# Performance work log

Measured on AMD Instinct MI355X. Metric: run time of the kernel, lower is better.

The kernel has to match this reference:

```python
import jax, jax.numpy as jnp
import numpy as np

H, D = 4, 32
EMB = H * D  # 128
COUNTS = [30000, 20000, 25000, 50000]  # pesticide, disease, plant, event
EDGE_TYPES = [(0, 1), (1, 0), (2, 1), (1, 2), (3, 0), (0, 3), (3, 2), (2, 3)]
E = 200000
INV_SQRT_D = 1.0 / float(np.sqrt(D))


def layer_norm(x, g, b, eps=1e-5):
    m = x.mean(-1, keepdims=True)
    v = ((x - m) ** 2).mean(-1, keepdims=True)
    return (x - m) * jax.lax.rsqrt(v + eps) * g + b


def hgt_block(xs, edges, kqvW, kqvb, outW, outb, skip, a_rel, m_rel, p_rel, ln_g, ln_b):
    # type-specific K/Q/V projections -> [N, H, D]
    K, Q, V = [], [], []
    for t in range(4):
        kqv = jnp.einsum('nc,kdc->knd', xs[t], kqvW[t]) + kqvb[t][:, None, :]
        K.append(kqv[0].reshape(-1, H, D))
        Q.append(kqv[1].reshape(-1, H, D))
        V.append(kqv[2].reshape(-1, H, D))
    per_dst = {t: [] for t in range(4)}
    for r, (s, t) in enumerate(EDGE_TYPES):
        src, dst = edges[r, 0], edges[r, 1]
        k_rel = jnp.einsum('ehd,hdf->ehf', K[s][src], a_rel[r])  # relation-specific key transform
        v_rel = jnp.einsum('ehd,hdf->ehf', V[s][src], m_rel[r])  # relation-specific message transform
        logit = (k_rel * Q[t][dst]).sum(-1) * p_rel[r] * INV_SQRT_D  # [E, H]
        per_dst[t].append((logit, v_rel, dst))
    outs = []
    for t in range(4):
        N = xs[t].shape[0]
        logits = jnp.concatenate([p[0] for p in per_dst[t]], axis=0)
        vals = jnp.concatenate([p[1] for p in per_dst[t]], axis=0)
        idx = jnp.concatenate([p[2] for p in per_dst[t]], axis=0)
        # single segment softmax per destination node across ALL incoming edge types (PyG HGTConv)
        mx = jax.ops.segment_max(logits, idx, num_segments=N)
        ex = jnp.exp(logits - mx[idx])
        den = jax.ops.segment_sum(ex, idx, num_segments=N)
        alpha = ex / jnp.maximum(den[idx], 1e-16)
        agg = jax.ops.segment_sum(vals * alpha[..., None], idx, num_segments=N).reshape(N, EMB)
        o = jax.nn.gelu(agg, approximate=False) @ outW[t].T + outb[t]
        sg = jax.nn.sigmoid(skip[t])
        o = sg * o + (1.0 - sg) * xs[t]  # HGTConv learnable skip
        # HGTBlock: residual add, LayerNorm, ReLU (dropout = identity in eval)
        outs.append(jax.nn.relu(layer_norm(o + xs[t], ln_g, ln_b)))
    return outs


def fusion(seq, inW, inb, outW, outb, g, b):
    # seq: [N, 3, EMB]; torch MultiheadAttention self-attention, then mean + LN
    qkv = seq @ inW.T + inb  # [N, 3, 3*EMB]
    q, k, v = jnp.split(qkv, 3, axis=-1)
    heads = lambda x: x.reshape(x.shape[0], 3, H, D).transpose(0, 2, 1, 3)  # [N,H,3,D]
    q, k, v = heads(q), heads(k), heads(v)
    att = jax.nn.softmax(jnp.einsum('nhqd,nhkd->nhqk', q, k) * INV_SQRT_D, axis=-1)
    o = jnp.einsum('nhqk,nhkd->nhqd', att, v).transpose(0, 2, 1, 3).reshape(-1, 3, EMB)
    o = o @ outW.T + outb
    return layer_norm(o.mean(axis=1), g, b)


def _forward(x_pest, x_dis, x_plant, edges, proj_W, proj_b, event_emb, kqv_W, kqv_b,
             out_W, out_b, skip, a_rel, m_rel, p_rel, blk_ln_g, blk_ln_b,
             fin_W, fin_b, fout_W, fout_b, f_ln_g, f_ln_b):
    xs = [jax.nn.relu(x_pest @ proj_W[0].T + proj_b[0]),
          jax.nn.relu(x_dis @ proj_W[1].T + proj_b[1]),
          jax.nn.relu(x_plant @ proj_W[2].T + proj_b[2]),
          event_emb]  # event_emb(arange(N)) == the full table
    layers = []
    cur = xs
    for l in range(3):
        cur = hgt_block(cur, edges, kqv_W[l], kqv_b[l], out_W[l], out_b[l], skip[l],
                        a_rel[l], m_rel[l], p_rel[l], blk_ln_g[l], blk_ln_b[l])
        layers.append(cur)
    outs = []
    for j, t in enumerate([0, 1, 2]):  # pesticide, disease, plant
        seq = jnp.stack([layers[0][t], layers[1][t], layers[2][t]], axis=1)
        outs.append(fusion(seq, fin_W[j], fin_b[j], fout_W[j], fout_b[j], f_ln_g[j], f_ln_b[j]))
    return jnp.concatenate(outs, axis=0)  # [30000+20000+25000, 128]


def setup_inputs() -> dict:
    key = jax.random.key(0)
    ks = iter(jax.random.split(key, 64))
    nrm = lambda shape, s=0.05: jax.random.normal(next(ks), shape, dtype=jnp.float32) * s
    rows = []
    for s, t in EDGE_TYPES:
        rows.append(jnp.stack([jax.random.randint(next(ks), (E,), 0, COUNTS[s]),
                               jax.random.randint(next(ks), (E,), 0, COUNTS[t])]))
    return {
        'x_pest': nrm((COUNTS[0], 64), 1.0),
        'x_dis': nrm((COUNTS[1], 64), 1.0),
        'x_plant': nrm((COUNTS[2], 64), 1.0),
        'edges': jnp.stack(rows).astype(jnp.int32),  # [8, 2, E]
        'proj_W': nrm((3, EMB, 64)), 'proj_b': nrm((3, EMB)),
        'event_emb': nrm((COUNTS[3], EMB), 1.0),
        'kqv_W': nrm((3, 4, 3, EMB, EMB)), 'kqv_b': nrm((3, 4, 3, EMB)),
        'out_W': nrm((3, 4, EMB, EMB)), 'out_b': nrm((3, 4, EMB)),
        'skip': nrm((3, 4), 1.0),
        'a_rel': nrm((3, 8, H, D, D), 0.1), 'm_rel': nrm((3, 8, H, D, D), 0.1),
        'p_rel': jnp.ones((3, 8, H), jnp.float32),
        'blk_ln_g': jnp.ones((3, EMB), jnp.float32), 'blk_ln_b': jnp.zeros((3, EMB), jnp.float32),
        'fin_W': nrm((3, 3 * EMB, EMB)), 'fin_b': nrm((3, 3 * EMB)),
        'fout_W': nrm((3, EMB, EMB)), 'fout_b': nrm((3, EMB)),
        'f_ln_g': jnp.ones((3, EMB), jnp.float32), 'f_ln_b': jnp.zeros((3, EMB), jnp.float32),
    }


def reference(x_pest, x_dis, x_plant, edges, proj_W, proj_b, event_emb, kqv_W, kqv_b,
              out_W, out_b, skip, a_rel, m_rel, p_rel, blk_ln_g, blk_ln_b,
              fin_W, fin_b, fout_W, fout_b, f_ln_g, f_ln_b):
    return _forward(x_pest, x_dis, x_plant, edges, proj_W, proj_b, event_emb, kqv_W, kqv_b,
                    out_W, out_b, skip, a_rel, m_rel, p_rel, blk_ln_g, blk_ln_b,
                    fin_W, fin_b, fout_W, fout_b, f_ln_g, f_ln_b)
```

## Files before the change

### kernel.cpp

```cpp
#include <hip/hip_runtime.h>
#include <math.h>

#define E_CNT 200000
typedef unsigned short bfu;
typedef unsigned short u16;
typedef __attribute__((ext_vector_type(8))) short bh8;
typedef __attribute__((ext_vector_type(4))) float f4;

__device__ __forceinline__ float gelu_f(float x) {
    return 0.5f * x * (1.0f + erff(x * 0.70710678118654752f));
}
__device__ __forceinline__ float bf2f(bfu u) { return __uint_as_float(((unsigned)u) << 16); }
__device__ __forceinline__ bfu f2bf(float f) {
    unsigned u = __float_as_uint(f);
    unsigned r = u + 0x7FFFu + ((u >> 16) & 1u);
    return (bfu)(r >> 16);
}
__device__ __forceinline__ int rsrc_of(int r) {
    const int a[8] = {0, 1, 2, 1, 3, 0, 3, 2}; return a[r];
}
__device__ __forceinline__ int rdst_of(int r) {
    const int a[8] = {1, 0, 1, 2, 0, 3, 2, 3}; return a[r];
}
__device__ __forceinline__ int rpoff_of(int r) {
    const int a[9] = {0, 20001, 50002, 70003, 95004, 125005, 175006, 200007, 250008};
    return a[r];
}

__global__ __launch_bounds__(256) void fill_val(float* p, int n, float v) {
    int i = blockIdx.x * 256 + threadIdx.x;
    if (i < n) p[i] = v;
}

__global__ __launch_bounds__(256) void cvt_pack(
    const float* __restrict__ out_W, const float* __restrict__ kqv_W,
    const float* __restrict__ fin_W, const float* __restrict__ fout_W,
    const float* __restrict__ event_emb,
    bfu* __restrict__ OWB, bfu* __restrict__ KWB, bfu* __restrict__ FINWB,
    bfu* __restrict__ FOUTWB, bfu* __restrict__ EVB)
{
    int i = blockIdx.x * 256 + threadIdx.x;
    const float* src; bfu* dst; size_t so, dox;
    if (i < 49152) { src = out_W; dst = OWB; so = (size_t)i * 4; dox = so; }
    else if (i < 98304) {
        int j = i - 49152; int m = j >> 12; int o = (j & 4095) * 4;
        src = kqv_W; dst = KWB;
        so = (size_t)m * 3 * 16384 + o; dox = (size_t)m * 16384 + o;
    }
    else if (i < 135168) { int j = i - 98304; src = fin_W; dst = FINWB; so = (size_t)j * 4; dox = so; }
    else if (i < 147456) { int j = i - 135168; src = fout_W; dst = FOUTWB; so = (size_t)j * 4; dox = so; }
    else if (i < 1747456) { int j = i - 147456; src = event_emb; dst = EVB; so = (size_t)j * 4; dox = so; }
    else return;
    float4 v = *(const float4*)(src + so);
    uint2 u;
    u.x = ((unsigned)f2bf(v.x)) | (((unsigned)f2bf(v.y)) << 16);
    u.y = ((unsigned)f2bf(v.z)) | (((unsigned)f2bf(v.w)) << 16);
    *(uint2*)(dst + dox) = u;
}

__global__ __launch_bounds__(256) void hist_all(const int* __restrict__ edges, int* __restrict__ rp) {
    int i = blockIdx.x * 256 + threadIdx.x;
    if (i >= 8 * E_CNT) return;
    int r = i / E_CNT, e = i - r * E_CNT;
    int d = edges[(size_t)(2 * r + 1) * E_CNT + e];
    atomicAdd(&rp[rpoff_of(r) + d + 1], 1);
}
__global__ __launch_bounds__(1024) void scan_part(int* __restrict__ a, int* __restrict__ part, int n) {
    __shared__ int lds[1024];
    int t = threadIdx.x, i = blockIdx.x * 1024 + t;
    int v = (i < n) ? a[i] : 0;
    lds[t] = v;
    __syncthreads();
    for (int off = 1; off < 1024; off <<= 1) {
        int u = (t >= off) ? lds[t - off] : 0;
        __syncthreads();
        lds[t] += u;
        __syncthreads();
    }
    if (i < n) a[i] = lds[t];
    if (t == 1023) part[blockIdx.x] = lds[1023];
}
__global__ __launch_bounds__(256) void scan_tot(int* __restrict__ part, int nb) {
    __shared__ int lds[256];
    int t = threadIdx.x;
    int v = (t < nb) ? part[t] : 0;
    lds[t] = v;
    __syncthreads();
    for (int off = 1; off < 256; off <<= 1) {
        int u = (t >= off) ? lds[t - off] : 0;
        __syncthreads();
        lds[t] += u;
        __syncthreads();
    }
    if (t < nb) part[t] = lds[t];
}
__global__ __launch_bounds__(1024) void scan_add(int* __restrict__ a, const int* __restrict__ part, int n) {
    int b = blockIdx.x + 1;
    int i = b * 1024 + threadIdx.x;
    if (i < n) a[i] += part[b - 1];
}
__global__ __launch_bounds__(256) void scatter_all(
    const int* __restrict__ edges, const int* __restrict__ RP,
    int* __restrict__ cur, u16* __restrict__ SIDX) {
    int i = blockIdx.x * 256 + threadIdx.x;
    if (i >= 8 * E_CNT) return;
    int r = i / E_CNT, e = i - r * E_CNT;
    int d = edges[(size_t)(2 * r + 1) * E_CNT + e];
    int pos = RP[rpoff_of(r) + d] + atomicAdd(&cur[r * 50000 + d], 1);
    SIDX[pos] = (u16)edges[(size_t)(2 * r) * E_CNT + e];
}

__global__ __launch_bounds__(256) void proj_gemm(
    const float* __restrict__ X, const float* __restrict__ W,
    const float* __restrict__ bias, bfu* __restrict__ Y, int N)
{
    __shared__ __align__(16) float Wt[32][132];
    __shared__ __align__(16) float Xt[32][36];
    const int tid = threadIdx.x;
    const int r0 = blockIdx.x * 32;
    const int rg = tid >> 5, cg = tid & 31;
    float acc[4][4];
    #pragma unroll
    for (int i = 0; i < 4; ++i)
        #pragma unroll
        for (int j = 0; j < 4; ++j) acc[i][j] = 0.f;
    for (int c0 = 0; c0 < 64; c0 += 32) {
        __syncthreads();
        #pragma unroll
        for (int k = 0; k < 4; ++k) {
            int v = tid + k * 256;
            int j = v >> 3, c4 = (v & 7) * 4;
            float4 w = *(const float4*)(W + (size_t)j * 64 + c0 + c4);
            Wt[c4 + 0][j] = w.x; Wt[c4 + 1][j] = w.y;
            Wt[c4 + 2][j] = w.z; Wt[c4 + 3][j] = w.w;
        }
        {
            int rr = tid >> 3, c4 = (tid & 7) * 4;
            int row = r0 + rr;
            float4 x = make_float4(0.f, 0.f, 0.f, 0.f);
            if (row < N) x = *(const float4*)(X + (size_t)row * 64 + c0 + c4);
            Xt[c4 + 0][rr] = x.x; Xt[c4 + 1][rr] = x.y;
            Xt[c4 + 2][rr] = x.z; Xt[c4 + 3][rr] = x.w;
        }
        __syncthreads();
        #pragma unroll
        for (int cc = 0; cc < 32; ++cc) {
            float4 xv = *(const float4*)(&Xt[cc][rg * 4]);
            float4 wv = *(const float4*)(&Wt[cc][cg * 4]);
            #pragma unroll
            for (int i = 0; i < 4; ++i) {
                float xs = (i == 0) ? xv.x : (i == 1) ? xv.y : (i == 2) ? xv.z : xv.w;
                acc[i][0] = fmaf(xs, wv.x, acc[i][0]);
                acc[i][1] = fmaf(xs, wv.y, acc[i][1]);
                acc[i][2] = fmaf(xs, wv.z, acc[i][2]);
                acc[i][3] = fmaf(xs, wv.w, acc[i][3]);
            }
        }
    }
    float4 bv = *(const float4*)(bias + cg * 4);
    #pragma unroll
    for (int ri = 0; ri < 4; ++ri) {
        int row = r0 + rg * 4 + ri;
        if (row >= N) continue;
        float y0 = fmaxf(acc[ri][0] + bv.x, 0.f);
        float y1 = fmaxf(acc[ri][1] + bv.y, 0.f);
        float y2 = fmaxf(acc[ri][2] + bv.z, 0.f);
        float y3 = fmaxf(acc[ri][3] + bv.w, 0.f);
        uint2 u;
        u.x = ((unsigned)f2bf(y0)) | (((unsigned)f2bf(y1)) << 16);
        u.y = ((unsigned)f2bf(y2)) | (((unsigned)f2bf(y3)) << 16);
        *(uint2*)(Y + (size_t)row * 128 + cg * 4) = u;
    }
}

__global__ __launch_bounds__(256) void build_rel(
    const float* __restrict__ kqvW_l, const float* __restrict__ kqvb_l,
    const float* __restrict__ a_l, const float* __restrict__ m_l,
    bfu* __restrict__ WQAB, float* __restrict__ BQA,
    bfu* __restrict__ WVMB, float* __restrict__ BVM)
{
    __shared__ float As[32][33];
    __shared__ float Ws[32][129];
    int tid = threadIdx.x;
    int b = blockIdx.x;
    if (b < 32) {
        int r = b >> 2, h = b & 3;
        int dt = rdst_of(r);
        const float* Wq = kqvW_l + ((size_t)dt * 3 + 1) * 16384;
        const float* bq = kqvb_l + ((size_t)dt * 3 + 1) * 128;
        const float* A = a_l + (size_t)r * 4096 + h * 1024;
        for (int v = tid; v < 1024; v += 256) As[v >> 5][v & 31] = A[v];
        for (int v = tid; v < 4096; v += 256)
            Ws[v >> 7][v & 127] = Wq[(size_t)(h * 32 + (v >> 7)) * 128 + (v & 127)];
        __syncthreads();
        int c = tid & 127, half = tid >> 7;
        for (int d = half; d < 32; d += 2) {
            float acc = 0.f;
            #pragma unroll
            for (int f = 0; f < 32; ++f) acc = fmaf(As[d][f], Ws[f][c], acc);
            WQAB[((size_t)r * 128 + h * 32 + d) * 128 + c] = f2bf(acc);
        }
        if (tid < 32) {
            int d = tid;
            float acc = 0.f;
            #pragma unroll
            for (int f = 0; f < 32; ++f) acc = fmaf(As[d][f], bq[h * 32 + f], acc);
            BQA[(size_t)r * 128 + h * 32 + d] = acc;
        }
    } else {
        int bb2 = b - 32;
        int r = bb2 >> 2, h = bb2 & 3;
        int st = rsrc_of(r);
        const float* Wv = kqvW_l + ((size_t)st * 3 + 2) * 16384;
        const float* bv = kqvb_l + ((size_t)st * 3 + 2) * 128;
        const float* M = m_l + (size_t)r * 4096 + h * 1024;
        for (int v = tid; v < 1024; v += 256) As[v >> 5][v & 31] = M[v];
        for (int v = tid; v < 4096; v += 256)
            Ws[v >> 7][v & 127] = Wv[(size_t)(h * 32 + (v >> 7)) * 128 + (v & 127)];
        __syncthreads();
        int c = tid & 127, half = tid >> 7;
        for (int f = half; f < 32; f += 2) {
            float acc = 0.f;
            #pragma unroll
            for (int d = 0; d < 32; ++d) acc = fmaf(As[d][f], Ws[d][c], acc);
            WVMB[((size_t)r * 128 + h * 32 + f) * 128 + c] = f2bf(acc);
        }
        if (tid < 32) {
            int f = tid;
            float acc = 0.f;
            #pragma unroll
            for (int d = 0; d < 32; ++d) acc = fmaf(As[d][f], bv[h * 32 + d], acc);
            BVM[(size_t)r * 128 + h * 32 + f] = acc;
        }
    }
}

struct GDesc { const bfu* X; const bfu* W; const float* bias; bfu* Y; int N; int ldy; int bend; };
struct GBatch { GDesc d[9]; };

__global__ __launch_bounds__(256) void mgemm_batch(GBatch gb) {
    int b = blockIdx.x;
    int gi = 0;
    #pragma unroll
    for (int k = 0; k < 8; ++k) gi += (b >= gb.d[k].bend) ? 1 : 0;
    const bfu* X = gb.d[0].X; const bfu* W = gb.d[0].W;
    const float* bi = gb.d[0].bias; bfu* Y = gb.d[0].Y;
    int N = gb.d[0].N, ldy = gb.d[0].ldy, bstart = 0;
    #pragma unroll
    for (int k = 1; k < 9; ++k) {
        if (gi == k) {
            X = gb.d[k].X; W = gb.d[k].W; bi = gb.d[k].bias; Y = gb.d[k].Y;
            N = gb.d[k].N; ldy = gb.d[k].ldy; bstart = gb.d[k - 1].bend;
        }
    }
    int bloc = b - bstart;
    const int tid = threadIdx.x;
    const int wave = tid >> 6, lane = tid & 63;
    const int row16 = lane & 15, kgrp = lane >> 4;
    const int r_base = bloc * 128 + wave * 32;
    f4 acc[2][8];
    #pragma unroll
    for (int t = 0; t < 2; ++t)
        #pragma unroll
        for (int n = 0; n < 8; ++n) acc[t][n] = (f4){0.f, 0.f, 0.f, 0.f};
    bh8 az = {0, 0, 0, 0, 0, 0, 0, 0};
    #pragma unroll
    for (int kb = 0; kb < 4; ++kb) {
        int ar0 = r_base + row16, ar1 = r_base + 16 + row16;
        bh8 a0 = az, a1 = az;
        if (ar0 < N) a0 = *(const bh8*)(X + (size_t)ar0 * 128 + kb * 32 + kgrp * 8);
        if (ar1 < N) a1 = *(const bh8*)(X + (size_t)ar1 * 128 + kb * 32 + kgrp * 8);
        #pragma unroll
        for (int n = 0; n < 8; ++n) {
            bh8 bv = *(const bh8*)(W + (size_t)(n * 16 + row16) * 128 + kb * 32 + kgrp * 8);
            acc[0][n] = __builtin_amdgcn_mfma_f32_16x16x32_bf16(a0, bv, acc[0][n], 0, 0, 0);
            acc[1][n] = __builtin_amdgcn_mfma_f32_16x16x32_bf16(a1, bv, acc[1][n], 0, 0, 0);
        }
    }
    #pragma unroll
    for (int t = 0; t < 2; ++t) {
        const int crow0 = r_base + t * 16 + kgrp * 4;
        #pragma unroll
        for (int n = 0; n < 8; ++n) {
            int col = n * 16 + row16;
            float bn = bi[col];
            #pragma unroll
            for (int j = 0; j < 4; ++j) {
                int row = crow0 + j;
                if (row < N) Y[(size_t)row * ldy + col] = f2bf(acc[t][n][j] + bn);
            }
        }
    }
}

__global__ __launch_bounds__(256) void agg_dual(
    const bfu* QAA, const bfu* __restrict__ QAB,
    const bfu* __restrict__ KA, const bfu* __restrict__ VMA,
    const bfu* __restrict__ KB, const bfu* __restrict__ VMB,
    const int* __restrict__ rpA, const int* __restrict__ rpB,
    const u16* __restrict__ sidx,
    const float* __restrict__ prlA, const float* __restrict__ prlB,
    bfu* ACC, int Nn)
{
    int n = blockIdx.x * 4 + (threadIdx.x >> 6);
    if (n >= Nn) return;
    int l = threadIdx.x & 63;
    int h = l >> 4;
    const float scl = 0.17677669529663687f;

    float m = -3.0e38f, d = 0.f, a0 = 0.f, a1 = 0.f;

    auto upd = [&](float s, unsigned vu) {
        float nm = fmaxf(m, s);
        float sc = __expf(m - nm), w = __expf(s - nm);
        d = d * sc + w;
        a0 = fmaf(w, bf2f((bfu)vu), a0 * sc);
        a1 = fmaf(w, bf2f((bfu)(vu >> 16)), a1 * sc);
        m = nm;
    };

    {
        unsigned qu = *(const unsigned*)(QAA + (size_t)n * 128 + 2 * l);
        float q0 = bf2f((bfu)qu), q1 = bf2f((bfu)(qu >> 16));
        float ph = prlA[h] * scl;
        int i = rpA[n], e1 = rpA[n + 1];
        for (; i + 1 < e1; i += 2) {
            int sa = sidx[i], sb = sidx[i + 1];
            unsigned ka = *(const unsigned*)(KA + (size_t)sa * 128 + 2 * l);
            unsigned kb = *(const unsigned*)(KA + (size_t)sb * 128 + 2 * l);
            unsigned va = *(const unsigned*)(VMA + (size_t)sa * 128 + 2 * l);
            unsigned vb = *(const unsigned*)(VMA + (size_t)sb * 128 + 2 * l);
            float s0 = fmaf(bf2f((bfu)ka), q0, bf2f((bfu)(ka >> 16)) * q1);
            float s1 = fmaf(bf2f((bfu)kb), q0, bf2f((bfu)(kb >> 16)) * q1);
            #pragma unroll
            for (int off = 1; off <= 8; off <<= 1) {
                s0 += __shfl_xor(s0, off);
                s1 += __shfl_xor(s1, off);
            }
            upd(s0 * ph, va);
            upd(s1 * ph, vb);
        }
        if (i < e1) {
            int sa = sidx[i];
            unsigned ka = *(const unsigned*)(KA + (size_t)sa * 128 + 2 * l);
            unsigned va = *(const unsigned*)(VMA + (size_t)sa * 128 + 2 * l);
            float s0 = fmaf(bf2f((bfu)ka), q0, bf2f((bfu)(ka >> 16)) * q1);
            #pragma unroll
            for (int off = 1; off <= 8; off <<= 1) s0 += __shfl_xor(s0, off);
            upd(s0 * ph, va);
        }
    }
    {
        unsigned qu = *(const unsigned*)(QAB + (size_t)n * 128 + 2 * l);
        float q0 = bf2f((bfu)qu), q1 = bf2f((bfu)(qu >> 16));
        float ph = prlB[h] * scl;
        int i = rpB[n], e1 = rpB[n + 1];
        for (; i + 1 < e1; i += 2) {
            int sa = sidx[i], sb = sidx[i + 1];
            unsigned ka = *(const unsigned*)(KB + (size_t)sa * 128 + 2 * l);
            unsigned kb = *(const unsigned*)(KB + (size_t)sb * 128 + 2 * l);
            unsigned va = *(const unsigned*)(VMB + (size_t)sa * 128 + 2 * l);
            unsigned vb = *(const unsigned*)(VMB + (size_t)sb * 128 + 2 * l);
            float s0 = fmaf(bf2f((bfu)ka), q0, bf2f((bfu)(ka >> 16)) * q1);
            float s1 = fmaf(bf2f((bfu)kb), q0, bf2f((bfu)(kb >> 16)) * q1);
            #pragma unroll
            for (int off = 1; off <= 8; off <<= 1) {
                s0 += __shfl_xor(s0, off);
                s1 += __shfl_xor(s1, off);
            }
            upd(s0 * ph, va);
            upd(s1 * ph, vb);
        }
        if (i < e1) {
            int sa = sidx[i];
            unsigned ka = *(const unsigned*)(KB + (size_t)sa * 128 + 2 * l);
            unsigned va = *(const unsigned*)(VMB + (size_t)sa * 128 + 2 * l);
            float s0 = fmaf(bf2f((bfu)ka), q0, bf2f((bfu)(ka >> 16)) * q1);
            #pragma unroll
            for (int off = 1; off <= 8; off <<= 1) s0 += __shfl_xor(s0, off);
            upd(s0 * ph, va);
        }
    }
    float rd = 1.f / fmaxf(d, 1e-16f);
    float y0 = gelu_f(a0 * rd);
    float y1 = gelu_f(a1 * rd);
    unsigned ou = ((unsigned)f2bf(y0)) | (((unsigned)f2bf(y1)) << 16);
    *(unsigned*)(ACC + (size_t)n * 128 + 2 * l) = ou;
}

__global__ __launch_bounds__(256) void mgemm_epi_layer(
    const bfu* __restrict__ A, const bfu* __restrict__ W, const float* __restrict__ bias,
    const bfu* __restrict__ Xr, const float* __restrict__ skp,
    const float* __restrict__ g, const float* __restrict__ bb,
    bfu* __restrict__ Y, int N)
{
    const int tid = threadIdx.x;
    const int wave = tid >> 6, lane = tid & 63;
    const int row16 = lane & 15, kgrp = lane >> 4;
    const int r_base = blockIdx.x * 64 + wave * 16;
    const int arow = r_base + row16;
    f4 acc[8];
    #pragma unroll
    for (int n = 0; n < 8; ++n) acc[n] = (f4){0.f, 0.f, 0.f, 0.f};
    bh8 az = {0, 0, 0, 0, 0, 0, 0, 0};
    #pragma unroll
    for (int kb = 0; kb < 4; ++kb) {
        bh8 a = az;
        if (arow < N) a = *(const bh8*)(A + (size_t)arow * 128 + kb * 32 + kgrp * 8);
        #pragma unroll
        for (int n = 0; n < 8; ++n) {
            bh8 bv = *(const bh8*)(W + (size_t)(n * 16 + row16) * 128 + kb * 32 + kgrp * 8);
            acc[n] = __builtin_amdgcn_mfma_f32_16x16x32_bf16(a, bv, acc[n], 0, 0, 0);
        }
    }
    const int crow0 = r_base + kgrp * 4;
    float sg = 1.f / (1.f + expf(-skp[0]));
    float z[8][4];
    #pragma unroll
    for (int n = 0; n < 8; ++n) {
        float bn = bias[n * 16 + row16];
        #pragma unroll
        for (int j = 0; j < 4; ++j) z[n][j] = acc[n][j] + bn;
    }
    #pragma unroll
    for (int j = 0; j < 4; ++j) {
        int row = crow0 + j;
        if (row >= N) continue;
        #pragma unroll
        for (int n = 0; n < 8; ++n) {
            float xr = bf2f(Xr[(size_t)row * 128 + n * 16 + row16]);
            z[n][j] = sg * z[n][j] + (1.f - sg) * xr + xr;
        }
    }
    float s[4], q[4];
    #pragma unroll
    for (int j = 0; j < 4; ++j) {
        s[j] = 0.f; q[j] = 0.f;
        #pragma unroll
        for (int n = 0; n < 8; ++n) { s[j] += z[n][j]; q[j] += z[n][j] * z[n][j]; }
    }
    #pragma unroll
    for (int off = 1; off <= 8; off <<= 1) {
        #pragma unroll
        for (int j = 0; j < 4; ++j) {
            s[j] += __shfl_xor(s[j], off);
            q[j] += __shfl_xor(q[j], off);
        }
    }
    #pragma unroll
    for (int j = 0; j < 4; ++j) {
        int row = crow0 + j;
        if (row >= N) continue;
        float mean = s[j] * (1.f / 128.f);
        float var = q[j] * (1.f / 128.f) - mean * mean;
        float inv = rsqrtf(var + 1e-5f);
        #pragma unroll
        for (int n = 0; n < 8; ++n) {
            int col = n * 16 + row16;
            float y = (z[n][j] - mean) * inv * g[col] + bb[col];
            Y[(size_t)row * 128 + col] = f2bf(fmaxf(y, 0.f));
        }
    }
}

__global__ __launch_bounds__(256) void mgemm_epi_ln(
    const bfu* __restrict__ X, const bfu* __restrict__ W, const float* __restrict__ bias,
    const float* __restrict__ g, const float* __restrict__ bb,
    float* __restrict__ Y, int N)
{
    const int tid = threadIdx.x;
    const int wave = tid >> 6, lane = tid & 63;
    const int row16 = lane & 15, kgrp = lane >> 4;
    const int r_base = blockIdx.x * 64 + wave * 16;
    const int arow = r_base + row16;
    f4 acc[8];
    #pragma unroll
    for (int n = 0; n < 8; ++n) acc[n] = (f4){0.f, 0.f, 0.f, 0.f};
    bh8 az = {0, 0, 0, 0, 0, 0, 0, 0};
    #pragma unroll
    for (int kb = 0; kb < 4; ++kb) {
        bh8 a = az;
        if (arow < N) a = *(const bh8*)(X + (size_t)arow * 128 + kb * 32 + kgrp * 8);
        #pragma unroll
        for (int n = 0; n < 8; ++n) {
            bh8 bv = *(const bh8*)(W + (size_t)(n * 16 + row16) * 128 + kb * 32 + kgrp * 8);
            acc[n] = __builtin_amdgcn_mfma_f32_16x16x32_bf16(a, bv, acc[n], 0, 0, 0);
        }
    }
    const int crow0 = r_base + kgrp * 4;
    float z[8][4];
    #pragma unroll
    for (int n = 0; n < 8; ++n) {
        float bn = bias[n * 16 + row16];
        #pragma unroll
        for (int j = 0; j < 4; ++j) z[n][j] = acc[n][j] + bn;
    }
    float s[4], q[4];
    #pragma unroll
    for (int j = 0; j < 4; ++j) {
        s[j] = 0.f; q[j] = 0.f;
        #pragma unroll
        for (int n = 0; n < 8; ++n) { s[j] += z[n][j]; q[j] += z[n][j] * z[n][j]; }
    }
    #pragma unroll
    for (int off = 1; off <= 8; off <<= 1) {
        #pragma unroll
        for (int j = 0; j < 4; ++j) {
            s[j] += __shfl_xor(s[j], off);
            q[j] += __shfl_xor(q[j], off);
        }
    }
    #pragma unroll
    for (int j = 0; j < 4; ++j) {
        int row = crow0 + j;
        if (row >= N) continue;
        float mean = s[j] * (1.f / 128.f);
        float var = q[j] * (1.f / 128.f) - mean * mean;
        float inv = rsqrtf(var + 1e-5f);
        #pragma unroll
        for (int n = 0; n < 8; ++n) {
            int col = n * 16 + row16;
            Y[(size_t)row * 128 + col] = (z[n][j] - mean) * inv * g[col] + bb[col];
        }
    }
}

__global__ __launch_bounds__(256) void attn_fuse(
    const bfu* __restrict__ QKV, bfu* __restrict__ OM, int M)
{
    int n = blockIdx.x * 4 + (threadIdx.x >> 6);
    int l = threadIdx.x & 63;
    if (n >= M) return;
    const bfu* base = QKV + (size_t)n * 1152;
    float q[3][2], k[3][2], v[3][2];
    #pragma unroll
    for (int p = 0; p < 3; ++p) {
        q[p][0] = bf2f(base[(0 * 3 + p) * 128 + l]);
        q[p][1] = bf2f(base[(0 * 3 + p) * 128 + l + 64]);
        k[p][0] = bf2f(base[(1 * 3 + p) * 128 + l]);
        k[p][1] = bf2f(base[(1 * 3 + p) * 128 + l + 64]);
        v[p][0] = bf2f(base[(2 * 3 + p) * 128 + l]);
        v[p][1] = bf2f(base[(2 * 3 + p) * 128 + l + 64]);
    }
    float lgA[3][3], lgB[3][3];
    #pragma unroll
    for (int qi = 0; qi < 3; ++qi)
        #pragma unroll
        for (int ki = 0; ki < 3; ++ki) {
            float s0 = q[qi][0] * k[ki][0];
            float s1 = q[qi][1] * k[ki][1];
            #pragma unroll
            for (int off = 1; off <= 16; off <<= 1) {
                s0 += __shfl_xor(s0, off);
                s1 += __shfl_xor(s1, off);
            }
            lgA[qi][ki] = s0 * 0.17677669529663687f;
            lgB[qi][ki] = s1 * 0.17677669529663687f;
        }
    float oA = 0.f, oB = 0.f;
    #pragma unroll
    for (int qi = 0; qi < 3; ++qi) {
        float mA = fmaxf(lgA[qi][0], fmaxf(lgA[qi][1], lgA[qi][2]));
        float e0 = __expf(lgA[qi][0] - mA), e1 = __expf(lgA[qi][1] - mA), e2 = __expf(lgA[qi][2] - mA);
        float rd = 1.f / (e0 + e1 + e2);
        oA += (e0 * v[0][0] + e1 * v[1][0] + e2 * v[2][0]) * rd;
        float mB = fmaxf(lgB[qi][0], fmaxf(lgB[qi][1], lgB[qi][2]));
        float f0 = __expf(lgB[qi][0] - mB), f1 = __expf(lgB[qi][1] - mB), f2 = __expf(lgB[qi][2] - mB);
        float rdB = 1.f / (f0 + f1 + f2);
        oB += (f0 * v[0][1] + f1 * v[1][1] + f2 * v[2][1]) * rdB;
    }
    OM[(size_t)n * 128 + l] = f2bf(oA * (1.f / 3.f));
    OM[(size_t)n * 128 + l + 64] = f2bf(oB * (1.f / 3.f));
}

extern "C" void kernel_launch(void* const* d_in, const int* in_sizes, int n_in,
                              void* d_out, int out_size, void* d_ws, size_t ws_size,
                              hipStream_t stream)
{
    const float* x_pest   = (const float*)d_in[0];
    const float* x_dis    = (const float*)d_in[1];
    const float* x_plant  = (const float*)d_in[2];
    const int*   edges    = (const int*)d_in[3];
    const float* proj_W   = (const float*)d_in[4];
    const float* proj_b   = (const float*)d_in[5];
    const float* event_emb= (const float*)d_in[6];
    const float* kqv_W    = (const float*)d_in[7];
    const float* kqv_b    = (const float*)d_in[8];
    const float* out_W    = (const float*)d_in[9];
    const float* out_b    = (const float*)d_in[10];
    const float* skip     = (const float*)d_in[11];
    const float* a_rel    = (const float*)d_in[12];
    const float* m_rel    = (const float*)d_in[13];
    const float* p_rel    = (const float*)d_in[14];
    const float* blk_ln_g = (const float*)d_in[15];
    const float* blk_ln_b = (const float*)d_in[16];
    const float* fin_W    = (const float*)d_in[17];
    const float* fin_b    = (const float*)d_in[18];
    const float* fout_W   = (const float*)d_in[19];
    const float* fout_b   = (const float*)d_in[20];
    const float* f_ln_g   = (const float*)d_in[21];
    const float* f_ln_b   = (const float*)d_in[22];
    float* out = (float*)d_out;

    static const int NT[4]  = {30000, 20000, 25000, 50000};
    static const int OFF[4] = {0, 30000, 50000, 75000};
    static const int RPOFF[9] = {0, 20001, 50002, 70003, 95004, 125005, 175006, 200007, 250008};
    static const int DG[4][2][2] = { {{1,1},{4,3}}, {{0,0},{2,2}}, {{3,1},{6,3}}, {{5,0},{7,2}} };

    char* wsb = (char*)d_ws;
    size_t ob = 0;
    auto alc = [&](size_t bytes) -> void* {
        void* p = wsb + ob; ob += (bytes + 255) & ~(size_t)255; return p;
    };
    bfu* LK0  = (bfu*)alc((size_t)75000 * 128 * 2);
    bfu* LK1  = (bfu*)alc((size_t)75000 * 128 * 2);
    bfu* POOL = (bfu*)alc((size_t)210000 * 128 * 2);
    bfu* WQAB = (bfu*)alc((size_t)8 * 16384 * 2);
    float* BQA = (float*)alc((size_t)8 * 128 * 4);
    bfu* WVMB = (bfu*)alc((size_t)8 * 16384 * 2);
    float* BVM = (float*)alc((size_t)8 * 128 * 4);
    bfu* KWB  = (bfu*)alc((size_t)12 * 16384 * 2);
    bfu* OWB  = (bfu*)alc((size_t)12 * 16384 * 2);
    bfu* FINWB = (bfu*)alc((size_t)3 * 49152 * 2);
    bfu* FOUTWB = (bfu*)alc((size_t)3 * 16384 * 2);
    int* RP   = (int*)alc((size_t)250008 * 4);
    int* PART = (int*)alc(1024);
    u16* SIDX = (u16*)alc((size_t)8 * E_CNT * 2);
    if (ws_size < ob) {
        fill_val<<<(out_size + 255) / 256, 256, 0, stream>>>(out, out_size, 1e30f);
        return;
    }
    int* CUR = (int*)POOL;
    bfu* QKVf = POOL;
    bfu* OMB  = POOL + (size_t)20000 * 1152;

    bfu* EVB = (bfu*)out;
    bfu* XB  = (bfu*)((char*)out + 12800000);
    bfu* L2F = (bfu*)((char*)out + 19200000);

    cvt_pack<<<(1747456 + 255) / 256, 256, 0, stream>>>(
        out_W, kqv_W, fin_W, fout_W, event_emb, OWB, KWB, FINWB, FOUTWB, EVB);

    hipMemsetAsync(RP, 0, (size_t)250008 * 4, stream);
    const int eg8 = (8 * E_CNT + 255) / 256;
    hist_all<<<eg8, 256, 0, stream>>>(edges, RP);
    scan_part<<<245, 1024, 0, stream>>>(RP, PART, 250008);
    scan_tot<<<1, 256, 0, stream>>>(PART, 245);
    scan_add<<<244, 1024, 0, stream>>>(RP, PART, 250008);
    hipMemsetAsync(CUR, 0, (size_t)8 * 50000 * 4, stream);
    scatter_all<<<eg8, 256, 0, stream>>>(edges, RP, CUR, SIDX);

    const float* xin0[3] = {x_pest, x_dis, x_plant};
    for (int t = 0; t < 3; ++t) {
        proj_gemm<<<(NT[t] + 31) / 32, 256, 0, stream>>>(
            xin0[t], proj_W + (size_t)t * 8192, proj_b + (size_t)t * 128,
            XB + (size_t)OFF[t] * 128, NT[t]);
    }

    auto launch_batch = [&](GDesc* ds, int cnt) {
        GBatch gb;
        int acc = 0;
        for (int i = 0; i < cnt; ++i) {
            gb.d[i] = ds[i];
            acc += (ds[i].N + 127) / 128;
            gb.d[i].bend = acc;
        }
        for (int i = cnt; i < 9; ++i) { gb.d[i] = gb.d[cnt - 1]; gb.d[i].bend = acc; }
        mgemm_batch<<<acc, 256, 0, stream>>>(gb);
    };

    for (int l = 0; l < 3; ++l) {
        const float* kqvW_l = kqv_W + (size_t)l * 12 * 16384;
        const float* kqvb_l = kqv_b + (size_t)l * 12 * 128;
        build_rel<<<64, 256, 0, stream>>>(kqvW_l, kqvb_l,
            a_rel + (size_t)l * 8 * 4096, m_rel + (size_t)l * 8 * 4096,
            WQAB, BQA, WVMB, BVM);

        auto feat_ptr = [&](int tt) -> const bfu* {
            if (tt == 3) return EVB;
            if (l == 0) return XB + (size_t)OFF[tt] * 128;
            return (l == 1 ? LK0 : LK1) + (size_t)OFF[tt] * 128;
        };

        int nord = (l == 2) ? 3 : 4;
        for (int dt = 0; dt < nord; ++dt) {
            int Ndt = NT[dt];
            int rA = DG[dt][0][0], sA = DG[dt][0][1];
            int rB = DG[dt][1][0], sB = DG[dt][1][1];
            int NsA = NT[sA], NsB = NT[sB];
            bfu* QA_A = POOL;
            bfu* QA_B = QA_A + (size_t)Ndt * 128;
            bfu* K_A  = QA_B + (size_t)Ndt * 128;
            bfu* VM_A = K_A + (size_t)NsA * 128;
            bfu* K_B  = VM_A + (size_t)NsA * 128;
            bfu* VM_B = K_B + (size_t)NsB * 128;

            GDesc ds[6];
            ds[0] = { feat_ptr(dt), WQAB + (size_t)rA * 16384, BQA + (size_t)rA * 128, QA_A, Ndt, 128, 0 };
            ds[1] = { feat_ptr(dt), WQAB + (size_t)rB * 16384, BQA + (size_t)rB * 128, QA_B, Ndt, 128, 0 };
            ds[2] = { feat_ptr(sA), KWB + (size_t)(l * 4 + sA) * 16384,
                      kqvb_l + ((size_t)sA * 3 + 0) * 128, K_A, NsA, 128, 0 };
            ds[3] = { feat_ptr(sA), WVMB + (size_t)rA * 16384, BVM + (size_t)rA * 128, VM_A, NsA, 128, 0 };
            ds[4] = { feat_ptr(sB), KWB + (size_t)(l * 4 + sB) * 16384,
                      kqvb_l + ((size_t)sB * 3 + 0) * 128, K_B, NsB, 128, 0 };
            ds[5] = { feat_ptr(sB), WVMB + (size_t)rB * 16384, BVM + (size_t)rB * 128, VM_B, NsB, 128, 0 };
            launch_batch(ds, 6);

            agg_dual<<<(Ndt + 3) / 4, 256, 0, stream>>>(
                QA_A, QA_B, K_A, VM_A, K_B, VM_B,
                RP + RPOFF[rA], RP + RPOFF[rB], SIDX,
                p_rel + (size_t)(l * 8 + rA) * 4, p_rel + (size_t)(l * 8 + rB) * 4,
                QA_A , Ndt);

            size_t wi = (size_t)l * 4 + dt;
            const bfu* xr = feat_ptr(dt);
            bfu* ydst = (dt == 3) ? EVB :
                        (l == 0 ? LK0 : (l == 1 ? LK1 : L2F)) + (size_t)OFF[dt] * 128;
            mgemm_epi_layer<<<(Ndt + 63) / 64, 256, 0, stream>>>(
                QA_A, OWB + wi * 16384, out_b + wi * 128, xr, skip + wi,
                blk_ln_g + (size_t)l * 128, blk_ln_b + (size_t)l * 128, ydst, Ndt);
        }
    }

    const int CH = 20000;
    for (int j = 0; j < 3; ++j) {
        int Nj = NT[j];
        for (int b0 = 0; b0 < Nj; b0 += CH) {
            int M = min(CH, Nj - b0);
            const bfu* srcs[3] = {
                LK0 + (size_t)(OFF[j] + b0) * 128,
                LK1 + (size_t)(OFF[j] + b0) * 128,
                L2F + (size_t)(OFF[j] + b0) * 128 };
            GDesc ds[9];
            int di = 0;
            for (int kk = 0; kk < 3; ++kk)
                for (int p = 0; p < 3; ++p) {
                    ds[di++] = { srcs[p], FINWB + (size_t)j * 49152 + (size_t)kk * 16384,
                                 fin_b + (size_t)j * 384 + kk * 128,
                                 QKVf + (size_t)(kk * 3 + p) * 128, M, 1152, 0 };
                }
            launch_batch(ds, 9);
            attn_fuse<<<(M + 3) / 4, 256, 0, stream>>>(QKVf, OMB, M);
            mgemm_epi_ln<<<(M + 63) / 64, 256, 0, stream>>>(
                OMB, FOUTWB + (size_t)j * 16384, fout_b + (size_t)j * 128,
                f_ln_g + (size_t)j * 128, f_ln_b + (size_t)j * 128,
                out + (size_t)(OFF[j] + b0) * 128, M);
        }
    }
}
```

Before: 1.802 ms.

## Batch input projections into one bf16 MFMA kernel and unroll edge loop by four

The three per-type fp32 LDS-tiled projection GEMMs become a single batched launch that uses bf16 MFMA 16x16x32, with proj_W converted to bf16 inside cvt_pack. The edge-attention kernel's two duplicated per-relation loops are folded into one lambda, and its gather loop is unrolled from two to four edges to raise memory-level parallelism. In exchange, X is rounded to bf16 before the projection, which adds precision loss, and the wider unroll raises register pressure.

After: 1.702 ms. 5.6% less time.

```diff
diff --git a/kernel.cpp b/kernel.cpp
--- a/kernel.cpp
+++ b/kernel.cpp
@@ -35,9 +35,9 @@
 __global__ __launch_bounds__(256) void cvt_pack(
     const float* __restrict__ out_W, const float* __restrict__ kqv_W,
     const float* __restrict__ fin_W, const float* __restrict__ fout_W,
-    const float* __restrict__ event_emb,
+    const float* __restrict__ event_emb, const float* __restrict__ proj_W,
     bfu* __restrict__ OWB, bfu* __restrict__ KWB, bfu* __restrict__ FINWB,
-    bfu* __restrict__ FOUTWB, bfu* __restrict__ EVB)
+    bfu* __restrict__ FOUTWB, bfu* __restrict__ EVB, bfu* __restrict__ PJWB)
 {
     int i = blockIdx.x * 256 + threadIdx.x;
     const float* src; bfu* dst; size_t so, dox;
@@ -50,6 +50,7 @@
     else if (i < 135168) { int j = i - 98304; src = fin_W; dst = FINWB; so = (size_t)j * 4; dox = so; }
     else if (i < 147456) { int j = i - 135168; src = fout_W; dst = FOUTWB; so = (size_t)j * 4; dox = so; }
     else if (i < 1747456) { int j = i - 147456; src = event_emb; dst = EVB; so = (size_t)j * 4; dox = so; }
+    else if (i < 1753600) { int j = i - 1747456; src = proj_W; dst = PJWB; so = (size_t)j * 4; dox = so; }
     else return;
     float4 v = *(const float4*)(src + so);
     uint2 u;
@@ -110,66 +111,71 @@
     SIDX[pos] = (u16)edges[(size_t)(2 * r) * E_CNT + e];
 }
 
-__global__ __launch_bounds__(256) void proj_gemm(
-    const float* __restrict__ X, const float* __restrict__ W,
-    const float* __restrict__ bias, bfu* __restrict__ Y, int N)
-{
-    __shared__ __align__(16) float Wt[32][132];
-    __shared__ __align__(16) float Xt[32][36];
+struct PDesc { const float* X; const bfu* W; const float* bias; bfu* Y; int N; int bend; };
+struct PBatch { PDesc d[3]; };
+
+__global__ __launch_bounds__(256) void mgemm_proj(PBatch pb) {
+    int b = blockIdx.x;
+    int gi = 0;
+    #pragma unroll
+    for (int k = 0; k < 2; ++k) gi += (b >= pb.d[k].bend) ? 1 : 0;
+    const float* X = pb.d[0].X; const bfu* W = pb.d[0].W;
+    const float* bi = pb.d[0].bias; bfu* Y = pb.d[0].Y;
+    int N = pb.d[0].N, bstart = 0;
+    #pragma unroll
+    for (int k = 1; k < 3; ++k) {
+        if (gi == k) {
+            X = pb.d[k].X; W = pb.d[k].W; bi = pb.d[k].bias; Y = pb.d[k].Y;
+            N = pb.d[k].N; bstart = pb.d[k - 1].bend;
+        }
+    }
+    int bloc = b - bstart;
     const int tid = threadIdx.x;
-    const int r0 = blockIdx.x * 32;
-    const int rg = tid >> 5, cg = tid & 31;
-    float acc[4][4];
-    #pragma unroll
-    for (int i = 0; i < 4; ++i)
-        #pragma unroll
-        for (int j = 0; j < 4; ++j) acc[i][j] = 0.f;
-    for (int c0 = 0; c0 < 64; c0 += 32) {
-        __syncthreads();
-        #pragma unroll
-        for (int k = 0; k < 4; ++k) {
-            int v = tid + k * 256;
-            int j = v >> 3, c4 = (v & 7) * 4;
-            float4 w = *(const float4*)(W + (size_t)j * 64 + c0 + c4);
-            Wt[c4 + 0][j] = w.x; Wt[c4 + 1][j] = w.y;
-            Wt[c4 + 2][j] = w.z; Wt[c4 + 3][j] = w.w;
-        }
-        {
-            int rr = tid >> 3, c4 = (tid & 7) * 4;
-            int row = r0 + rr;
-            float4 x = make_float4(0.f, 0.f, 0.f, 0.f);
-            if (row < N) x = *(const float4*)(X + (size_t)row * 64 + c0 + c4);
-            Xt[c4 + 0][rr] = x.x; Xt[c4 + 1][rr] = x.y;
-            Xt[c4 + 2][rr] = x.z; Xt[c4 + 3][rr] = x.w;
-        }
-        __syncthreads();
-        #pragma unroll
-        for (int cc = 0; cc < 32; ++cc) {
-            float4 xv = *(const float4*)(&Xt[cc][rg * 4]);
-            float4 wv = *(const float4*)(&Wt[cc][cg * 4]);
-            #pragma unroll
-            for (int i = 0; i < 4; ++i) {
-                float xs = (i == 0) ? xv.x : (i == 1) ? xv.y : (i == 2) ? xv.z : xv.w;
-                acc[i][0] = fmaf(xs, wv.x, acc[i][0]);
-                acc[i][1] = fmaf(xs, wv.y, acc[i][1]);
-                acc[i][2] = fmaf(xs, wv.z, acc[i][2]);
-                acc[i][3] = fmaf(xs, wv.w, acc[i][3]);
+    const int wave = tid >> 6, lane = tid & 63;
+    const int row16 = lane & 15, kgrp = lane >> 4;
+    const int r_base = bloc * 128 + wave * 32;
+    f4 acc[2][8];
+    #pragma unroll
+    for (int t = 0; t < 2; ++t)
+        #pragma unroll
+        for (int n = 0; n < 8; ++n) acc[t][n] = (f4){0.f, 0.f, 0.f, 0.f};
+    bh8 az = {0, 0, 0, 0, 0, 0, 0, 0};
+    #pragma unroll
+    for (int kb = 0; kb < 2; ++kb) {
+        bh8 a[2] = {az, az};
+        #pragma unroll
+        for (int t = 0; t < 2; ++t) {
+            int ar = r_base + t * 16 + row16;
+            if (ar < N) {
+                const float* xp = X + (size_t)ar * 64 + kb * 32 + kgrp * 8;
+                float4 xa = *(const float4*)xp;
+                float4 xb = *(const float4*)(xp + 4);
+                a[t][0] = (short)f2bf(xa.x); a[t][1] = (short)f2bf(xa.y);
+                a[t][2] = (short)f2bf(xa.z); a[t][3] = (short)f2bf(xa.w);
+                a[t][4] = (short)f2bf(xb.x); a[t][5] = (short)f2bf(xb.y);
+                a[t][6] = (short)f2bf(xb.z); a[t][7] = (short)f2bf(xb.w);
             }
         }
-    }
-    float4 bv = *(const float4*)(bias + cg * 4);
-    #pragma unroll
-    for (int ri = 0; ri < 4; ++ri) {
-        int row = r0 + rg * 4 + ri;
-        if (row >= N) continue;
-        float y0 = fmaxf(acc[ri][0] + bv.x, 0.f);
-        float y1 = fmaxf(acc[ri][1] + bv.y, 0.f);
-        float y2 = fmaxf(acc[ri][2] + bv.z, 0.f);
-        float y3 = fmaxf(acc[ri][3] + bv.w, 0.f);
-        uint2 u;
-        u.x = ((unsigned)f2bf(y0)) | (((unsigned)f2bf(y1)) << 16);
-        u.y = ((unsigned)f2bf(y2)) | (((unsigned)f2bf(y3)) << 16);
-        *(uint2*)(Y + (size_t)row * 128 + cg * 4) = u;
+        #pragma unroll
+        for (int n = 0; n < 8; ++n) {
+            bh8 bv = *(const bh8*)(W + (size_t)(n * 16 + row16) * 64 + kb * 32 + kgrp * 8);
+            acc[0][n] = __builtin_amdgcn_mfma_f32_16x16x32_bf16(a[0], bv, acc[0][n], 0, 0, 0);
+            acc[1][n] = __builtin_amdgcn_mfma_f32_16x16x32_bf16(a[1], bv, acc[1][n], 0, 0, 0);
+        }
+    }
+    #pragma unroll
+    for (int t = 0; t < 2; ++t) {
+        const int crow0 = r_base + t * 16 + kgrp * 4;
+        #pragma unroll
+        for (int n = 0; n < 8; ++n) {
+            int col = n * 16 + row16;
+            float bn = bi[col];
+            #pragma unroll
+            for (int j = 0; j < 4; ++j) {
+                int row = crow0 + j;
+                if (row < N) Y[(size_t)row * 128 + col] = f2bf(fmaxf(acc[t][n][j] + bn, 0.f));
+            }
+        }
     }
 }
 
@@ -319,68 +325,51 @@
         m = nm;
     };
 
-    {
-        unsigned qu = *(const unsigned*)(QAA + (size_t)n * 128 + 2 * l);
+    auto rel = [&](const bfu* QA, const bfu* __restrict__ K, const bfu* __restrict__ VM,
+                   const int* __restrict__ rp, const float* __restrict__ prl) {
+        unsigned qu = *(const unsigned*)(QA + (size_t)n * 128 + 2 * l);
         float q0 = bf2f((bfu)qu), q1 = bf2f((bfu)(qu >> 16));
-        float ph = prlA[h] * scl;
-        int i = rpA[n], e1 = rpA[n + 1];
-        for (; i + 1 < e1; i += 2) {
-            int sa = sidx[i], sb = sidx[i + 1];
-            unsigned ka = *(const unsigned*)(KA + (size_t)sa * 128 + 2 * l);
-            unsigned kb = *(const unsigned*)(KA + (size_t)sb * 128 + 2 * l);
-            unsigned va = *(const unsigned*)(VMA + (size_t)sa * 128 + 2 * l);
-            unsigned vb = *(const unsigned*)(VMA + (size_t)sb * 128 + 2 * l);
+        float ph = prl[h] * scl;
+        int i = rp[n], e1 = rp[n + 1];
+        for (; i + 3 < e1; i += 4) {
+            int sa = sidx[i], sb = sidx[i + 1], sc2 = sidx[i + 2], sd = sidx[i + 3];
+            unsigned ka = *(const unsigned*)(K + (size_t)sa * 128 + 2 * l);
+            unsigned kb = *(const unsigned*)(K + (size_t)sb * 128 + 2 * l);
+            unsigned kc = *(const unsigned*)(K + (size_t)sc2 * 128 + 2 * l);
+            unsigned kd = *(const unsigned*)(K + (size_t)sd * 128 + 2 * l);
+            unsigned va = *(const unsigned*)(VM + (size_t)sa * 128 + 2 * l);
+            unsigned vb = *(const unsigned*)(VM + (size_t)sb * 128 + 2 * l);
+            unsigned vc = *(const unsigned*)(VM + (size_t)sc2 * 128 + 2 * l);
+            unsigned vd = *(const unsigned*)(VM + (size_t)sd * 128 + 2 * l);
             float s0 = fmaf(bf2f((bfu)ka), q0, bf2f((bfu)(ka >> 16)) * q1);
             float s1 = fmaf(bf2f((bfu)kb), q0, bf2f((bfu)(kb >> 16)) * q1);
+            float s2 = fmaf(bf2f((bfu)kc), q0, bf2f((bfu)(kc >> 16)) * q1);
+            float s3 = fmaf(bf2f((bfu)kd), q0, bf2f((bfu)(kd >> 16)) * q1);
             #pragma unroll
             for (int off = 1; off <= 8; off <<= 1) {
                 s0 += __shfl_xor(s0, off);
                 s1 += __shfl_xor(s1, off);
+                s2 += __shfl_xor(s2, off);
+                s3 += __shfl_xor(s3, off);
             }
             upd(s0 * ph, va);
             upd(s1 * ph, vb);
-        }
-        if (i < e1) {
+            upd(s2 * ph, vc);
+            upd(s3 * ph, vd);
+        }
+        for (; i < e1; ++i) {
             int sa = sidx[i];
-            unsigned ka = *(const unsigned*)(KA + (size_t)sa * 128 + 2 * l);
-            unsigned va = *(const unsigned*)(VMA + (size_t)sa * 128 + 2 * l);
+            unsigned ka = *(const unsigned*)(K + (size_t)sa * 128 + 2 * l);
+            unsigned va = *(const unsigned*)(VM + (size_t)sa * 128 + 2 * l);
             float s0 = fmaf(bf2f((bfu)ka), q0, bf2f((bfu)(ka >> 16)) * q1);
             #pragma unroll
             for (int off = 1; off <= 8; off <<= 1) s0 += __shfl_xor(s0, off);
             upd(s0 * ph, va);
         }
-    }
-    {
-        unsigned qu = *(const unsigned*)(QAB + (size_t)n * 128 + 2 * l);
-        float q0 = bf2f((bfu)qu), q1 = bf2f((bfu)(qu >> 16));
-        float ph = prlB[h] * scl;
-        int i = rpB[n], e1 = rpB[n + 1];
-        for (; i + 1 < e1; i += 2) {
-            int sa = sidx[i], sb = sidx[i + 1];
-            unsigned ka = *(const unsigned*)(KB + (size_t)sa * 128 + 2 * l);
-            unsigned kb = *(const unsigned*)(KB + (size_t)sb * 128 + 2 * l);
-            unsigned va = *(const unsigned*)(VMB + (size_t)sa * 128 + 2 * l);
-            unsigned vb = *(const unsigned*)(VMB + (size_t)sb * 128 + 2 * l);
-            float s0 = fmaf(bf2f((bfu)ka), q0, bf2f((bfu)(ka >> 16)) * q1);
-            float s1 = fmaf(bf2f((bfu)kb), q0, bf2f((bfu)(kb >> 16)) * q1);
-            #pragma unroll
-            for (int off = 1; off <= 8; off <<= 1) {
-                s0 += __shfl_xor(s0, off);
-                s1 += __shfl_xor(s1, off);
-            }
-            upd(s0 * ph, va);
-            upd(s1 * ph, vb);
-        }
-        if (i < e1) {
-            int sa = sidx[i];
-            unsigned ka = *(const unsigned*)(KB + (size_t)sa * 128 + 2 * l);
-            unsigned va = *(const unsigned*)(VMB + (size_t)sa * 128 + 2 * l);
-            float s0 = fmaf(bf2f((bfu)ka), q0, bf2f((bfu)(ka >> 16)) * q1);
-            #pragma unroll
-            for (int off = 1; off <= 8; off <<= 1) s0 += __shfl_xor(s0, off);
-            upd(s0 * ph, va);
-        }
-    }
+    };
+    rel(QAA, KA, VMA, rpA, prlA);
+    rel(QAB, KB, VMB, rpB, prlB);
+
     float rd = 1.f / fmaxf(d, 1e-16f);
     float y0 = gelu_f(a0 * rd);
     float y1 = gelu_f(a1 * rd);
@@ -623,6 +612,7 @@
     bfu* OWB  = (bfu*)alc((size_t)12 * 16384 * 2);
     bfu* FINWB = (bfu*)alc((size_t)3 * 49152 * 2);
     bfu* FOUTWB = (bfu*)alc((size_t)3 * 16384 * 2);
+    bfu* PJWB = (bfu*)alc((size_t)3 * 8192 * 2);
     int* RP   = (int*)alc((size_t)250008 * 4);
     int* PART = (int*)alc(1024);
     u16* SIDX = (u16*)alc((size_t)8 * E_CNT * 2);
@@ -638,8 +628,9 @@
     bfu* XB  = (bfu*)((char*)out + 12800000);
     bfu* L2F = (bfu*)((char*)out + 19200000);
 
-    cvt_pack<<<(1747456 + 255) / 256, 256, 0, stream>>>(
-        out_W, kqv_W, fin_W, fout_W, event_emb, OWB, KWB, FINWB, FOUTWB, EVB);
+    cvt_pack<<<(1753600 + 255) / 256, 256, 0, stream>>>(
+        out_W, kqv_W, fin_W, fout_W, event_emb, proj_W,
+        OWB, KWB, FINWB, FOUTWB, EVB, PJWB);
 
     hipMemsetAsync(RP, 0, (size_t)250008 * 4, stream);
     const int eg8 = (8 * E_CNT + 255) / 256;
@@ -650,11 +641,20 @@
     hipMemsetAsync(CUR, 0, (size_t)8 * 50000 * 4, stream);
     scatter_all<<<eg8, 256, 0, stream>>>(edges, RP, CUR, SIDX);
 
-    const float* xin0[3] = {x_pest, x_dis, x_plant};
-    for (int t = 0; t < 3; ++t) {
-        proj_gemm<<<(NT[t] + 31) / 32, 256, 0, stream>>>(
-            xin0[t], proj_W + (size_t)t * 8192, proj_b + (size_t)t * 128,
-            XB + (size_t)OFF[t] * 128, NT[t]);
+    {
+        PBatch pb;
+        const float* xin0[3] = {x_pest, x_dis, x_plant};
+        int acc = 0;
+        for (int t = 0; t < 3; ++t) {
+            pb.d[t].X = xin0[t];
+            pb.d[t].W = PJWB + (size_t)t * 8192;
+            pb.d[t].bias = proj_b + (size_t)t * 128;
+            pb.d[t].Y = XB + (size_t)OFF[t] * 128;
+            pb.d[t].N = NT[t];
+            acc += (NT[t] + 127) / 128;
+            pb.d[t].bend = acc;
+        }
+        mgemm_proj<<<acc, 256, 0, stream>>>(pb);
     }
 
     auto launch_batch = [&](GDesc* ds, int cnt) {
```
